# Optimization experiments

Measured on AMD Instinct MI355X. Metric: run time of the kernel, lower is better.

## Reference

```python
import jax, jax.numpy as jnp
import numpy as np

TEMPERATURE = 0.07
BASE_TEMPERATURE = 0.07


def _supcon_one(feat, labels):
    # feat: [B, V, D], labels: [B]  (contrast_mode='all')
    B, V, D = feat.shape
    N = V * B
    # torch.cat(torch.unbind(feat, dim=1), dim=0): view-major ordering
    contrast = jnp.swapaxes(feat, 0, 1).reshape(N, D)  # [N, D]
    logits = jnp.einsum('nd,md->nm', contrast, contrast) / TEMPERATURE  # [N, N]
    # subtract detached row max for numerical stability
    logits = logits - jax.lax.stop_gradient(jnp.max(logits, axis=1, keepdims=True))
    pos = (labels[:, None] == labels[None, :]).astype(feat.dtype)  # [B, B]
    mask = jnp.tile(pos, (V, V))                                   # [N, N]
    logits_mask = 1.0 - jnp.eye(N, dtype=feat.dtype)               # zero out self-contrast
    mask = mask * logits_mask
    exp_logits = jnp.exp(logits) * logits_mask
    log_prob = logits - jnp.log(exp_logits.sum(axis=1, keepdims=True))
    mean_log_prob_pos = (mask * log_prob).sum(axis=1) / mask.sum(axis=1)
    return -(TEMPERATURE / BASE_TEMPERATURE) * mean_log_prob_pos.mean()


def setup_inputs() -> dict:
    key = jax.random.key(0)
    k1, k2 = jax.random.split(key)
    feat = jax.random.normal(k1, (16, 1024, 2, 128), dtype=jnp.float32)
    feat = feat / jnp.linalg.norm(feat, axis=-1, keepdims=True)  # unit-norm embeddings
    labels = jax.random.randint(k2, (16, 1024), 0, 64)
    return {"features": feat, "labels": labels}


def reference(features, labels):
    # vmap over the outer batch dim (replaces the Python loop), then mean
    losses = jax.vmap(_supcon_one)(features, labels)
    return losses.mean()
```

## Files before the change

kernel.cpp:

```cpp
#include <hip/hip_runtime.h>
#include <hip/hip_bf16.h>

#define TEMP_INV 14.285714285714286f
#define KL2E     20.60992947626f
#define NC2      (-20.60992947626f)
#define NROWS 2048
#define DDIM 128

typedef __attribute__((ext_vector_type(8))) short bf16x8;
typedef __attribute__((ext_vector_type(4))) float f32x4;

#define GLOAD16(g, l) \
  __builtin_amdgcn_global_load_lds((const __attribute__((address_space(1))) void*)(g), \
                                   (__attribute__((address_space(3))) void*)(l), 16, 0, 0)

__global__ __launch_bounds__(256) void cast_reorder_kernel(
    const float* __restrict__ feat, __hip_bfloat16* __restrict__ out)
{
    int t = blockIdx.x * blockDim.x + threadIdx.x;
    int e = t << 2;
    int d = e & 127;
    int v = (e >> 7) & 1;
    int i = (e >> 8) & 1023;
    int b = e >> 18;
    const float4 f = *reinterpret_cast<const float4*>(feat + e);
    union { __hip_bfloat16 h[4]; uint2 u; } o;
    o.h[0] = __float2bfloat16(f.x);
    o.h[1] = __float2bfloat16(f.y);
    o.h[2] = __float2bfloat16(f.z);
    o.h[3] = __float2bfloat16(f.w);
    size_t oe = (size_t)(((b << 11) + (v << 10) + i)) * DDIM + d;
    *reinterpret_cast<uint2*>(out + oe) = o.u;
}

__global__ __launch_bounds__(256, 4) void supcon_main_kernel(
    const __hip_bfloat16* __restrict__ contrast,
    const int* __restrict__ labels,
    float* __restrict__ rsum_ws, float* __restrict__ ps_ws, float* __restrict__ sd_ws)
{
    __shared__ __align__(16) char wbuf[4][2][4096];
    __shared__ int slab[1024];

    const int tid  = threadIdx.x;
    const int lane = tid & 63;
    const int w    = tid >> 6;
    const int hi   = lane >> 4;
    const int lo   = lane & 15;

    const int bid = blockIdx.x;
    const int xcd = bid & 7, idx = bid >> 3;
    const int b   = xcd * 2 + (idx >> 6);
    const int rem = idx & 63;
    const int rb  = rem >> 1, ch = rem & 1;
    const int n0  = rb * 64;
    const int wr0 = n0 + w * 16;
    const int cb0 = ch * 1024;

    const __hip_bfloat16* cbase = contrast + (size_t)b * NROWS * DDIM;
    const int* lb = labels + b * 1024;

    #pragma unroll
    for (int it = 0; it < 4; ++it) slab[it * 256 + tid] = lb[it * 256 + tid];

    char* buf0 = &wbuf[w][0][0];

    #pragma unroll
    for (int i = 0; i < 4; ++i) {
        const int r = 4 * i + hi;
        GLOAD16(cbase + (size_t)(wr0 + r) * DDIM + ((lo ^ (r & 7)) << 3),
                buf0 + i * 1024);
    }
    asm volatile("s_waitcnt vmcnt(0)" ::: "memory");
    __builtin_amdgcn_sched_barrier(0);

    bf16x8 afrag[4];
    int boff[4];
    #pragma unroll
    for (int ks = 0; ks < 4; ++ks) {
        boff[ks] = lo * 256 + (((hi + 4 * ks) ^ (lo & 7)) << 4);
        afrag[ks] = *reinterpret_cast<const bf16x8*>(buf0 + boff[ks]);
    }
    __syncthreads();

    int nrow[4], rlab[4];
    #pragma unroll
    for (int j = 0; j < 4; ++j) {
        nrow[j] = wr0 + hi * 4 + j;
        rlab[j] = slab[nrow[j] & 1023];
    }

    const __hip_bfloat16* gsrc[4];
    #pragma unroll
    for (int i = 0; i < 4; ++i) {
        const int r = 4 * i + hi;
        gsrc[i] = cbase + (size_t)(cb0 + r) * DDIM + ((lo ^ (r & 7)) << 3);
    }
    #pragma unroll
    for (int i = 0; i < 4; ++i) GLOAD16(gsrc[i], buf0 + i * 1024);
    #pragma unroll
    for (int i = 0; i < 4; ++i) GLOAD16(gsrc[i] + 16 * DDIM, buf0 + 4096 + i * 1024);
    #pragma unroll
    for (int i = 0; i < 4; ++i) gsrc[i] += 32 * DDIM;

    float se[4] = {0, 0, 0, 0}, ps[4] = {0, 0, 0, 0}, sdg[4] = {0, 0, 0, 0};
    const int sd_step = (wr0 - cb0) >> 4;

    for (int s = 0; s < 64; ++s) {
        char* cur = buf0 + ((s & 1) << 12);
        asm volatile("s_waitcnt vmcnt(4)" ::: "memory");
        __builtin_amdgcn_sched_barrier(0);

        bf16x8 bf[4];
        #pragma unroll
        for (int ks = 0; ks < 4; ++ks)
            bf[ks] = *reinterpret_cast<const bf16x8*>(cur + boff[ks]);

        f32x4 acc = {0.f, 0.f, 0.f, 0.f};
        #pragma unroll
        for (int ks = 0; ks < 4; ++ks)
            acc = __builtin_amdgcn_mfma_f32_16x16x32_bf16(afrag[ks], bf[ks], acc, 0, 0, 0);

        #pragma unroll
        for (int i = 0; i < 4; ++i) { GLOAD16(gsrc[i], cur + i * 1024); gsrc[i] += 16 * DDIM; }
        if (s == 61) {
            #pragma unroll
            for (int i = 0; i < 4; ++i) gsrc[i] -= 64 * 16 * DDIM;
        }

        const int lm = slab[s * 16 + lo];
        #pragma unroll
        for (int j = 0; j < 4; ++j) {
            const float v = acc[j];
            se[j] += exp2f(fmaf(v, KL2E, NC2));
            ps[j] += (lm == rlab[j]) ? v : 0.f;
        }
        if (s == sd_step) {
            const int m = cb0 + s * 16 + lo;
            #pragma unroll
            for (int j = 0; j < 4; ++j)
                if (m == nrow[j]) sdg[j] = acc[j];
        }
    }

    #pragma unroll
    for (int j = 0; j < 4; ++j) {
        float s = se[j], P = ps[j], D = sdg[j];
        #pragma unroll
        for (int o = 1; o < 16; o <<= 1) {
            s += __shfl_xor(s, o);
            P += __shfl_xor(P, o);
            D += __shfl_xor(D, o);
        }
        if (lo == 0) {
            const int gn = b * NROWS + nrow[j];
            atomicAdd(&rsum_ws[gn], s);
            atomicAdd(&ps_ws[gn], P);
            atomicAdd(&sd_ws[gn], D);
        }
    }
}

__global__ __launch_bounds__(256) void finalize_kernel(
    const int* __restrict__ labels,
    const float* __restrict__ rsum_ws, const float* __restrict__ ps_ws,
    const float* __restrict__ sd_ws, float* __restrict__ out)
{
    __shared__ int cnt_s[64];
    __shared__ float wred[4];
    const int tid = threadIdx.x, lane = tid & 63, wv = tid >> 6;
    const int gid = blockIdx.x * 256 + tid;
    const int b = gid >> 11, n = gid & 2047;
    const int* lb = labels + b * 1024;

    if (tid < 64) cnt_s[tid] = 0;
    __syncthreads();
    #pragma unroll
    for (int k = 0; k < 4; ++k) atomicAdd(&cnt_s[lb[tid * 4 + k]], 1);
    __syncthreads();

    const int l = lb[n & 1023];
    const float poscnt = (float)(2 * cnt_s[l] - 1);
    const float D  = sd_ws[gid];
    const float P  = ps_ws[gid] - D;
    const float rs = rsum_ws[gid] - exp2f(fmaf(D, KL2E, NC2));
    float mlpp = P * TEMP_INV / poscnt - TEMP_INV - __logf(rs);

    #pragma unroll
    for (int o = 1; o < 64; o <<= 1) mlpp += __shfl_xor(mlpp, o);
    if (lane == 0) wred[wv] = mlpp;
    __syncthreads();
    if (tid == 0)
        atomicAdd(out, -(wred[0] + wred[1] + wred[2] + wred[3]) * (1.0f / 32768.0f));
}

extern "C" void kernel_launch(void* const* d_in, const int* in_sizes, int n_in,
                              void* d_out, int out_size, void* d_ws, size_t ws_size,
                              hipStream_t stream) {
    const float* feat = (const float*)d_in[0];
    const int* labels = (const int*)d_in[1];
    float* out = (float*)d_out;

    char* ws = (char*)d_ws;
    __hip_bfloat16* contrast = (__hip_bfloat16*)ws;
    float* rsum_ws = (float*)(ws + 8388608);
    float* ps_ws   = (float*)(ws + 8519680);
    float* sd_ws   = (float*)(ws + 8650752);

    hipMemsetAsync(d_out, 0, sizeof(float), stream);
    hipMemsetAsync(ws + 8388608, 0, 3 * 131072, stream);
    cast_reorder_kernel<<<4096, 256, 0, stream>>>(feat, contrast);
    supcon_main_kernel<<<1024, 256, 0, stream>>>(contrast, labels, rsum_ws, ps_ws, sd_ws);
    finalize_kernel<<<128, 256, 0, stream>>>(labels, rsum_ws, ps_ws, sd_ws, out);
}
```

Baseline: 119.5 us.

## Compute positive sums via per-label feature sums and enlarge main GEMM tile

The positive-pair logit sum is rewritten algebraically as a dot product between each row and the per-label sum of feature vectors. A new lsum kernel builds those sums and the finalize kernel computes them together with the self-similarity, so the main kernel only accumulates the exp row sums. The main kernel also moves to 128-row by 512-column block tiles, with shared B tiles double-buffered across waves and two A fragments per wave, which raises MFMA reuse per B load. This adds a kernel launch, LDS atomics in lsum, and a small numeric difference because the positive sums no longer come from bf16 GEMM outputs.

```diff
diff --git a/kernel.cpp b/kernel.cpp
--- a/kernel.cpp
+++ b/kernel.cpp
@@ -33,156 +33,200 @@
     *reinterpret_cast<uint2*>(out + oe) = o.u;
 }
 
+__global__ __launch_bounds__(256) void lsum_kernel(
+    const __hip_bfloat16* __restrict__ contrast,
+    const int* __restrict__ labels, float* __restrict__ Lsum)
+{
+    __shared__ float Ls[64 * 128];
+    const int tid = threadIdx.x;
+    const int b = blockIdx.x >> 3, seg = blockIdx.x & 7;
+    for (int k = tid; k < 8192; k += 256) Ls[k] = 0.f;
+    __syncthreads();
+    const int half = tid >> 7, d = tid & 127;
+    const int* lb = labels + b * 1024;
+    const __hip_bfloat16* cb = contrast + (size_t)b * NROWS * DDIM;
+    for (int it = 0; it < 128; ++it) {
+        const int row = seg * 256 + it * 2 + half;
+        const int lab = lb[row & 1023];
+        const float v = __bfloat162float(cb[(size_t)row * DDIM + d]);
+        atomicAdd(&Ls[lab * 128 + d], v);
+    }
+    __syncthreads();
+    float* Lg = Lsum + b * 8192;
+    for (int k = tid; k < 8192; k += 256) atomicAdd(&Lg[k], Ls[k]);
+}
+
 __global__ __launch_bounds__(256, 4) void supcon_main_kernel(
     const __hip_bfloat16* __restrict__ contrast,
-    const int* __restrict__ labels,
-    float* __restrict__ rsum_ws, float* __restrict__ ps_ws, float* __restrict__ sd_ws)
-{
-    __shared__ __align__(16) char wbuf[4][2][4096];
-    __shared__ int slab[1024];
+    float* __restrict__ rsum_ws)
+{
+    __shared__ __align__(16) char lds[2][16384];
 
     const int tid  = threadIdx.x;
     const int lane = tid & 63;
     const int w    = tid >> 6;
-    const int hi   = lane >> 4;
-    const int lo   = lane & 15;
+    const int hi   = lane >> 4, lo = lane & 15;
 
     const int bid = blockIdx.x;
     const int xcd = bid & 7, idx = bid >> 3;
     const int b   = xcd * 2 + (idx >> 6);
     const int rem = idx & 63;
-    const int rb  = rem >> 1, ch = rem & 1;
-    const int n0  = rb * 64;
-    const int wr0 = n0 + w * 16;
-    const int cb0 = ch * 1024;
+    const int rb  = rem >> 2;
+    const int cs  = rem & 3;
 
     const __hip_bfloat16* cbase = contrast + (size_t)b * NROWS * DDIM;
-    const int* lb = labels + b * 1024;
-
-    #pragma unroll
-    for (int it = 0; it < 4; ++it) slab[it * 256 + tid] = lb[it * 256 + tid];
-
-    char* buf0 = &wbuf[w][0][0];
-
+
+    {
+        char* abuf = (w < 2) ? &lds[0][0] : &lds[1][0];
+        #pragma unroll
+        for (int i = 0; i < 8; ++i) {
+            const int cg  = w * 8 + i;
+            const int row = cg * 4 + hi;
+            const int lc  = (w & 1) * 8 + i;
+            GLOAD16(cbase + (size_t)(rb * 128 + row) * DDIM + ((lo ^ (row & 7)) << 3),
+                    abuf + lc * 1024);
+        }
+    }
+    asm volatile("s_waitcnt vmcnt(0)\ns_barrier" ::: "memory");
+
+    bf16x8 afrag[2][4];
+    {
+        const char* abase = (w < 2) ? &lds[0][0] : &lds[1][0];
+        #pragma unroll
+        for (int fr = 0; fr < 2; ++fr) {
+            const int lr = (w & 1) * 32 + fr * 16 + lo;
+            #pragma unroll
+            for (int ks = 0; ks < 4; ++ks) {
+                const int q = ks * 4 + hi;
+                afrag[fr][ks] = *reinterpret_cast<const bf16x8*>(
+                    abase + lr * 256 + ((q ^ (lo & 7)) << 4));
+            }
+        }
+    }
+    asm volatile("s_waitcnt lgkmcnt(0)\ns_barrier" ::: "memory");
+
+    const __hip_bfloat16* gsrcB[4];
     #pragma unroll
     for (int i = 0; i < 4; ++i) {
-        const int r = 4 * i + hi;
-        GLOAD16(cbase + (size_t)(wr0 + r) * DDIM + ((lo ^ (r & 7)) << 3),
-                buf0 + i * 1024);
-    }
-    asm volatile("s_waitcnt vmcnt(0)" ::: "memory");
-    __builtin_amdgcn_sched_barrier(0);
-
-    bf16x8 afrag[4];
-    int boff[4];
-    #pragma unroll
-    for (int ks = 0; ks < 4; ++ks) {
-        boff[ks] = lo * 256 + (((hi + 4 * ks) ^ (lo & 7)) << 4);
-        afrag[ks] = *reinterpret_cast<const bf16x8*>(buf0 + boff[ks]);
-    }
-    __syncthreads();
-
-    int nrow[4], rlab[4];
-    #pragma unroll
-    for (int j = 0; j < 4; ++j) {
-        nrow[j] = wr0 + hi * 4 + j;
-        rlab[j] = slab[nrow[j] & 1023];
-    }
-
-    const __hip_bfloat16* gsrc[4];
+        const int row = (w * 4 + i) * 4 + hi;
+        gsrcB[i] = cbase + (size_t)(cs * 512 + row) * DDIM + ((lo ^ (row & 7)) << 3);
+    }
     #pragma unroll
     for (int i = 0; i < 4; ++i) {
-        const int r = 4 * i + hi;
-        gsrc[i] = cbase + (size_t)(cb0 + r) * DDIM + ((lo ^ (r & 7)) << 3);
-    }
-    #pragma unroll
-    for (int i = 0; i < 4; ++i) GLOAD16(gsrc[i], buf0 + i * 1024);
-    #pragma unroll
-    for (int i = 0; i < 4; ++i) GLOAD16(gsrc[i] + 16 * DDIM, buf0 + 4096 + i * 1024);
-    #pragma unroll
-    for (int i = 0; i < 4; ++i) gsrc[i] += 32 * DDIM;
-
-    float se[4] = {0, 0, 0, 0}, ps[4] = {0, 0, 0, 0}, sdg[4] = {0, 0, 0, 0};
-    const int sd_step = (wr0 - cb0) >> 4;
-
-    for (int s = 0; s < 64; ++s) {
-        char* cur = buf0 + ((s & 1) << 12);
-        asm volatile("s_waitcnt vmcnt(4)" ::: "memory");
-        __builtin_amdgcn_sched_barrier(0);
-
-        bf16x8 bf[4];
-        #pragma unroll
-        for (int ks = 0; ks < 4; ++ks)
-            bf[ks] = *reinterpret_cast<const bf16x8*>(cur + boff[ks]);
-
-        f32x4 acc = {0.f, 0.f, 0.f, 0.f};
-        #pragma unroll
-        for (int ks = 0; ks < 4; ++ks)
-            acc = __builtin_amdgcn_mfma_f32_16x16x32_bf16(afrag[ks], bf[ks], acc, 0, 0, 0);
-
-        #pragma unroll
-        for (int i = 0; i < 4; ++i) { GLOAD16(gsrc[i], cur + i * 1024); gsrc[i] += 16 * DDIM; }
-        if (s == 61) {
-            #pragma unroll
-            for (int i = 0; i < 4; ++i) gsrc[i] -= 64 * 16 * DDIM;
-        }
-
-        const int lm = slab[s * 16 + lo];
+        GLOAD16(gsrcB[i], &lds[0][0] + (w * 4 + i) * 1024);
+        gsrcB[i] += 64 * DDIM;
+    }
+
+    int bro[4];
+    #pragma unroll
+    for (int ks = 0; ks < 4; ++ks)
+        bro[ks] = lo * 256 + (((ks * 4 + hi) ^ (lo & 7)) << 4);
+
+    float se[2][4] = {{0,0,0,0},{0,0,0,0}};
+
+    #pragma unroll
+    for (int p = 0; p < 8; ++p) {
+        const int cur = p & 1;
+        if (p < 7) {
+            char* nbuf = &lds[cur ^ 1][0];
+            #pragma unroll
+            for (int i = 0; i < 4; ++i) {
+                GLOAD16(gsrcB[i], nbuf + (w * 4 + i) * 1024);
+                gsrcB[i] += 64 * DDIM;
+            }
+            asm volatile("s_waitcnt vmcnt(4)\ns_barrier" ::: "memory");
+        } else {
+            asm volatile("s_waitcnt vmcnt(0)\ns_barrier" ::: "memory");
+        }
+        const char* base = &lds[cur][0];
+
+        f32x4 acc[2][4];
+        #pragma unroll
+        for (int fr = 0; fr < 2; ++fr)
+            #pragma unroll
+            for (int fc = 0; fc < 4; ++fc)
+                acc[fr][fc] = (f32x4){0.f, 0.f, 0.f, 0.f};
+
+        #pragma unroll
+        for (int fc = 0; fc < 4; ++fc) {
+            bf16x8 bf[4];
+            #pragma unroll
+            for (int ks = 0; ks < 4; ++ks)
+                bf[ks] = *reinterpret_cast<const bf16x8*>(base + fc * 4096 + bro[ks]);
+            #pragma unroll
+            for (int ks = 0; ks < 4; ++ks) {
+                acc[0][fc] = __builtin_amdgcn_mfma_f32_16x16x32_bf16(
+                    afrag[0][ks], bf[ks], acc[0][fc], 0, 0, 0);
+                acc[1][fc] = __builtin_amdgcn_mfma_f32_16x16x32_bf16(
+                    afrag[1][ks], bf[ks], acc[1][fc], 0, 0, 0);
+            }
+        }
+
+        #pragma unroll
+        for (int fr = 0; fr < 2; ++fr)
+            #pragma unroll
+            for (int fc = 0; fc < 4; ++fc)
+                #pragma unroll
+                for (int j = 0; j < 4; ++j)
+                    se[fr][j] += exp2f(fmaf(acc[fr][fc][j], KL2E, NC2));
+
+        asm volatile("s_barrier" ::: "memory");
+    }
+
+    #pragma unroll
+    for (int fr = 0; fr < 2; ++fr)
         #pragma unroll
         for (int j = 0; j < 4; ++j) {
-            const float v = acc[j];
-            se[j] += exp2f(fmaf(v, KL2E, NC2));
-            ps[j] += (lm == rlab[j]) ? v : 0.f;
-        }
-        if (s == sd_step) {
-            const int m = cb0 + s * 16 + lo;
-            #pragma unroll
-            for (int j = 0; j < 4; ++j)
-                if (m == nrow[j]) sdg[j] = acc[j];
-        }
-    }
-
-    #pragma unroll
-    for (int j = 0; j < 4; ++j) {
-        float s = se[j], P = ps[j], D = sdg[j];
-        #pragma unroll
-        for (int o = 1; o < 16; o <<= 1) {
-            s += __shfl_xor(s, o);
-            P += __shfl_xor(P, o);
-            D += __shfl_xor(D, o);
-        }
-        if (lo == 0) {
-            const int gn = b * NROWS + nrow[j];
-            atomicAdd(&rsum_ws[gn], s);
-            atomicAdd(&ps_ws[gn], P);
-            atomicAdd(&sd_ws[gn], D);
-        }
-    }
+            float s = se[fr][j];
+            s += __shfl_xor(s, 1); s += __shfl_xor(s, 2);
+            s += __shfl_xor(s, 4); s += __shfl_xor(s, 8);
+            if (lo == 0)
+                atomicAdd(&rsum_ws[b * NROWS + rb * 128 + w * 32 + fr * 16 + hi * 4 + j], s);
+        }
 }
 
 __global__ __launch_bounds__(256) void finalize_kernel(
+    const __hip_bfloat16* __restrict__ contrast,
     const int* __restrict__ labels,
-    const float* __restrict__ rsum_ws, const float* __restrict__ ps_ws,
-    const float* __restrict__ sd_ws, float* __restrict__ out)
+    const float* __restrict__ rsum_ws, const float* __restrict__ Lsum,
+    float* __restrict__ out)
 {
     __shared__ int cnt_s[64];
     __shared__ float wred[4];
     const int tid = threadIdx.x, lane = tid & 63, wv = tid >> 6;
-    const int gid = blockIdx.x * 256 + tid;
-    const int b = gid >> 11, n = gid & 2047;
+    const int b = blockIdx.x >> 4;
+    const int rloc = (blockIdx.x & 15) * 128 + (tid >> 1);
+    const int half = tid & 1;
     const int* lb = labels + b * 1024;
 
     if (tid < 64) cnt_s[tid] = 0;
     __syncthreads();
-    #pragma unroll
-    for (int k = 0; k < 4; ++k) atomicAdd(&cnt_s[lb[tid * 4 + k]], 1);
-    __syncthreads();
-
-    const int l = lb[n & 1023];
-    const float poscnt = (float)(2 * cnt_s[l] - 1);
-    const float D  = sd_ws[gid];
-    const float P  = ps_ws[gid] - D;
-    const float rs = rsum_ws[gid] - exp2f(fmaf(D, KL2E, NC2));
+    for (int k = tid; k < 1024; k += 256) atomicAdd(&cnt_s[lb[k]], 1);
+    __syncthreads();
+
+    const int lab = lb[rloc & 1023];
+    const __hip_bfloat16* crow = contrast + ((size_t)b * NROWS + rloc) * DDIM + half * 64;
+    const float* L = Lsum + b * 8192 + lab * 128 + half * 64;
+
+    float psum = 0.f, sd = 0.f;
+    #pragma unroll
+    for (int k = 0; k < 8; ++k) {
+        bf16x8 cv = *reinterpret_cast<const bf16x8*>(crow + k * 8);
+        #pragma unroll
+        for (int e = 0; e < 8; ++e) {
+            union { short s; unsigned short u; } uu; uu.s = cv[e];
+            unsigned int bits = ((unsigned int)uu.u) << 16;
+            float c; __builtin_memcpy(&c, &bits, 4);
+            psum = fmaf(c, L[k * 8 + e], psum);
+            sd   = fmaf(c, c, sd);
+        }
+    }
+    psum += __shfl_xor(psum, 1);
+    sd   += __shfl_xor(sd, 1);
+
+    const float poscnt = (float)(2 * cnt_s[lab] - 1);
+    const float P  = psum - sd;
+    const float rs = rsum_ws[b * NROWS + rloc] - exp2f(fmaf(sd, KL2E, NC2));
     float mlpp = P * TEMP_INV / poscnt - TEMP_INV - __logf(rs);
 
     #pragma unroll
@@ -190,7 +234,7 @@
     if (lane == 0) wred[wv] = mlpp;
     __syncthreads();
     if (tid == 0)
-        atomicAdd(out, -(wred[0] + wred[1] + wred[2] + wred[3]) * (1.0f / 32768.0f));
+        atomicAdd(out, -(wred[0] + wred[1] + wred[2] + wred[3]) * (1.0f / 65536.0f));
 }
 
 extern "C" void kernel_launch(void* const* d_in, const int* in_sizes, int n_in,
@@ -203,12 +247,12 @@
     char* ws = (char*)d_ws;
     __hip_bfloat16* contrast = (__hip_bfloat16*)ws;
     float* rsum_ws = (float*)(ws + 8388608);
-    float* ps_ws   = (float*)(ws + 8519680);
-    float* sd_ws   = (float*)(ws + 8650752);
+    float* Lsum_ws = (float*)(ws + 8519680);
 
     hipMemsetAsync(d_out, 0, sizeof(float), stream);
-    hipMemsetAsync(ws + 8388608, 0, 3 * 131072, stream);
+    hipMemsetAsync(ws + 8388608, 0, 131072 + 524288, stream);
     cast_reorder_kernel<<<4096, 256, 0, stream>>>(feat, contrast);
-    supcon_main_kernel<<<1024, 256, 0, stream>>>(contrast, labels, rsum_ws, ps_ws, sd_ws);
-    finalize_kernel<<<128, 256, 0, stream>>>(labels, rsum_ws, ps_ws, sd_ws, out);
-}
+    lsum_kernel<<<128, 256, 0, stream>>>(contrast, labels, Lsum_ws);
+    supcon_main_kernel<<<1024, 256, 0, stream>>>(contrast, rsum_ws);
+    finalize_kernel<<<256, 256, 0, stream>>>(contrast, labels, rsum_ws, Lsum_ws, out);
+}
```

Result: slower. 230.6 us (+92.9%).
